# Kernel tuning notes

Measured on AMD Instinct MI355X. Metric: run time of the kernel, lower is better.

The kernel has to match this reference:

```python
import jax, jax.numpy as jnp
import numpy as np
from jax import lax

B, R, C, K = 4, 512, 80, 100          # images, rois/img, fg classes, post_nms_top_k
NMS_TH, SCORE_TH = 0.3, 0.1
MEAN = jnp.zeros(4, jnp.float32)       # delta_mean
STD = jnp.ones(4, jnp.float32)         # delta_std
NEG = jnp.float32(-1e9)
DWH_CLIP = jnp.float32(4.135166556742356)  # log(1000/16), standard bbox_xform clip


def setup_inputs() -> dict:
    key = jax.random.key(0)
    k1, k2, k3, k4 = jax.random.split(key, 4)
    x1y1 = jax.random.uniform(k1, (B, R, 2), minval=0.0, maxval=800.0)
    wh = jax.random.uniform(k2, (B, R, 2), minval=16.0, maxval=220.0)
    batch_rois = jnp.concatenate([x1y1, jnp.minimum(x1y1 + wh, 1023.0)], axis=-1)
    bbox_score = jax.random.uniform(k3, (B * R, C + 1, 1, 1), dtype=jnp.float32)
    bbox_deltas = jax.random.normal(k4, (B * R, (C + 1) * 4, 1, 1), dtype=jnp.float32) * 0.2
    im_hw = jnp.full((B, 1, 1, 2), 1024, dtype=jnp.int32)
    return {"batch_rois": batch_rois, "bbox_score": bbox_score,
            "bbox_deltas": bbox_deltas, "im_hw": im_hw}


def _pairwise_iou(b):
    # b: [R, 4] (x1,y1,x2,y2) -> [R, R]
    area = (b[:, 2] - b[:, 0]) * (b[:, 3] - b[:, 1])
    lt = jnp.maximum(b[:, None, :2], b[None, :, :2])
    rb = jnp.minimum(b[:, None, 2:], b[None, :, 2:])
    wh = jnp.maximum(rb - lt, 0.0)
    inter = wh[..., 0] * wh[..., 1]
    return inter / (area[:, None] + area[None, :] - inter + 1e-9)


def _nms_one_class(boxes, scores):
    # boxes: [R,4], scores: [R] -> keep mask + score-sorted boxes/scores
    order = jnp.argsort(-scores)
    b = boxes[order]
    s = scores[order]
    iou = _pairwise_iou(b)  # [R, R]

    def body(sup, i):
        keep_i = jnp.logical_and(jnp.logical_not(sup[i]), s[i] > SCORE_TH)
        new = jnp.where(keep_i, jnp.logical_or(sup, iou[i] > NMS_TH), sup)
        new = new.at[i].set(sup[i])  # never self-suppress
        return new, keep_i

    _, keep = lax.scan(body, jnp.zeros(b.shape[0], bool), jnp.arange(b.shape[0]))
    return keep, b, s


def _decode(rois, deltas, hw):
    # rois: [R,4], deltas: [R,C,4], hw: [2] (h, w) -> decoded boxes [R,C,4]
    d = deltas * STD + MEAN
    w = rois[:, 2] - rois[:, 0]
    h = rois[:, 3] - rois[:, 1]
    cx = rois[:, 0] + 0.5 * w
    cy = rois[:, 1] + 0.5 * h
    dx, dy = d[..., 0], d[..., 1]
    dw = jnp.minimum(d[..., 2], DWH_CLIP)
    dh = jnp.minimum(d[..., 3], DWH_CLIP)
    pcx = dx * w[:, None] + cx[:, None]
    pcy = dy * h[:, None] + cy[:, None]
    pw = w[:, None] * jnp.exp(dw)
    ph = h[:, None] * jnp.exp(dh)
    x1 = jnp.clip(pcx - 0.5 * pw, 0.0, hw[1] - 1.0)
    y1 = jnp.clip(pcy - 0.5 * ph, 0.0, hw[0] - 1.0)
    x2 = jnp.clip(pcx + 0.5 * pw, 0.0, hw[1] - 1.0)
    y2 = jnp.clip(pcy + 0.5 * ph, 0.0, hw[0] - 1.0)
    return jnp.stack([x1, y1, x2, y2], axis=-1)


def reference(batch_rois, bbox_score, bbox_deltas, im_hw):
    scores = bbox_score.reshape(B, R, C + 1)[..., 1:]               # [B,R,C] (skip bg)
    deltas = bbox_deltas.reshape(B, R, C + 1, 4)[:, :, 1:, :]       # [B,R,C,4]
    hw = im_hw.reshape(B, 2).astype(jnp.float32)

    def per_image(rois, sc, dl, hw_i):
        boxes = _decode(rois, dl, hw_i)                              # [R,C,4]
        keep, bs, ss = jax.vmap(_nms_one_class)(
            jnp.swapaxes(boxes, 0, 1), sc.T)                         # [C,R]...
        cls = jnp.broadcast_to(jnp.arange(C, dtype=jnp.float32)[:, None], (C, R))
        flat_s = jnp.where(keep, ss, NEG).reshape(-1)                # [C*R]
        top_s, idx = lax.top_k(flat_s, K)
        tb = bs.reshape(-1, 4)[idx]
        tc = cls.reshape(-1)[idx]
        valid = top_s > NEG * 0.5
        row = jnp.concatenate([tb, top_s[:, None], tc[:, None]], axis=-1)  # [K,6]
        pad = jnp.concatenate([jnp.zeros((K, 5), jnp.float32),
                               -jnp.ones((K, 1), jnp.float32)], axis=-1)
        return jnp.where(valid[:, None], row, pad)

    return jax.vmap(per_image)(batch_rois, scores, deltas, hw)      # [B,K,6]
```

## Files before the change

### kernel.cpp

```cpp
#include <hip/hip_runtime.h>
#include <cstdint>

#define BB 4
#define RR 512
#define CC 80
#define KK 100
#define NMS_TH 0.3f
#define SCORE_TH 0.1f
#define DWH_CLIP 4.135166556742356f

typedef unsigned short u16;
typedef unsigned int u32;
typedef unsigned long long u64;

__device__ __forceinline__ u32 f32_sortable(float f) {
  u32 u = __float_as_uint(f);
  u32 mask = (u32)((int)u >> 31) | 0x80000000u;
  return u ^ mask;
}
__device__ __forceinline__ float sortable_to_f32(u32 s) {
  u32 u = (s & 0x80000000u) ? (s ^ 0x80000000u) : ~s;
  return __uint_as_float(u);
}

__global__ __launch_bounds__(512) void nms_fused(
    const float* __restrict__ rois,
    const float* __restrict__ scores,
    const float* __restrict__ deltas,
    const int*   __restrict__ im_hw,
    u64*   __restrict__ cand_key,
    float4* __restrict__ cand_box)
{
#pragma clang fp contract(off)
  const int bc = blockIdx.x;
  const int b = bc / CC, c = bc % CC;
  const int tid = threadIdx.x;
  const int lane = tid & 63, wv = tid >> 6;

  __shared__ u64    keyarr[2 * RR];
  __shared__ float4 box_s[RR];
  __shared__ float  sco_s[RR];
  __shared__ u64    rmk_w[8 * 64];
  __shared__ u64    supacc_arr[8];
  __shared__ float4 kbox[KK];
  __shared__ float  ksc[KK];
  __shared__ float  karea[KK];
  __shared__ int    nkept_s;

  const float fh = (float)im_hw[b * 2 + 0] - 1.0f;
  const float fw = (float)im_hw[b * 2 + 1] - 1.0f;

  {
    const float sc = scores[(b * RR + tid) * (CC + 1) + (c + 1)];
    u64 v = ((u64)(~f32_sortable(sc)) << 32) | (u32)tid;
    const u32 t = (u32)tid;
    u32 pp = 0;
    for (u32 kk = 2; kk <= RR; kk <<= 1) {
      for (u32 j = kk >> 1; j > 0; j >>= 1) {
        u64 p;
        if (j >= 64) {
          u64* buf = keyarr + (pp & 1) * RR;
          buf[t] = v;
          __syncthreads();
          p = buf[t ^ j];
          ++pp;
        } else {
          p = __shfl_xor(v, (int)j);
        }
        bool up = ((t & kk) == 0);
        bool lower = ((t & j) == 0);
        bool takemin = (up == lower);
        bool pless = (p < v);
        v = (takemin == pless) ? p : v;
      }
    }
    keyarr[t] = v;
  }
  __syncthreads();

  {
    const u64 kv = keyarr[tid];
    const int r = (int)(kv & 0xFFFFFFFFull);
    const float sc = sortable_to_f32(~(u32)(kv >> 32));
    const float4 roi = *(const float4*)&rois[(b * RR + r) * 4];
    const int base = (b * RR + r) * (CC + 1) + (c + 1);
    const float4 d = *(const float4*)&deltas[base * 4];

    float w  = roi.z - roi.x;
    float h  = roi.w - roi.y;
    float cx = roi.x + 0.5f * w;
    float cy = roi.y + 0.5f * h;
    float dw = fminf(d.z, DWH_CLIP);
    float dh = fminf(d.w, DWH_CLIP);
    float pcx = d.x * w + cx;
    float pcy = d.y * h + cy;
    float pw = w * expf(dw);
    float ph = h * expf(dh);
    float hx = 0.5f * pw, hy = 0.5f * ph;
    float x1 = fminf(fmaxf(pcx - hx, 0.0f), fw);
    float y1 = fminf(fmaxf(pcy - hy, 0.0f), fh);
    float x2 = fminf(fmaxf(pcx + hx, 0.0f), fw);
    float y2 = fminf(fmaxf(pcy + hy, 0.0f), fh);

    box_s[tid] = make_float4(x1, y1, x2, y2);
    sco_s[tid] = sc;
    if (tid == 0) nkept_s = 0;
  }
  __syncthreads();

  int nk = 0;
  for (int w = 0; w < 8 && nk < KK; ++w) {
    const float4 bxc = box_s[w * 64 + lane];
    const float ar = (bxc.z - bxc.x) * (bxc.w - bxc.y);
    const float areps = ar + 1e-9f;

    {
      float4 cb[8]; float ca[8]; float inA[8];
      #pragma unroll
      for (int jj = 0; jj < 8; ++jj) {
        cb[jj] = box_s[w * 64 + wv * 8 + jj];
        ca[jj] = (cb[jj].z - cb[jj].x) * (cb[jj].w - cb[jj].y);
      }
      u64 myrow = 0;
      u32 unca = 0;
      #pragma unroll
      for (int jj = 0; jj < 8; ++jj) {
        float iw = fminf(bxc.z, cb[jj].z) - fmaxf(bxc.x, cb[jj].x);
        float ih = fminf(bxc.w, cb[jj].w) - fmaxf(bxc.y, cb[jj].y);
        iw = fmaxf(iw, 0.0f);
        ih = fmaxf(ih, 0.0f);
        const float inter = iw * ih;
        inA[jj] = inter;
        const float S = ca[jj] + areps;
        const bool yes = inter * 4.3333247f > S;
        const bool no  = inter * 4.3333420f < S;
        myrow |= yes ? (1ull << jj) : 0ull;
        unca  |= (!(yes || no)) ? (1u << jj) : 0u;
      }
      if (__any(unca != 0)) {
        #pragma unroll
        for (int jj = 0; jj < 8; ++jj) {
          const float denom = ((ca[jj] + ar) - inA[jj]) + 1e-9f;
          const bool pe = inA[jj] / denom > NMS_TH;
          const u64 bit = 1ull << jj;
          if (unca & (1u << jj)) myrow = pe ? (myrow | bit) : (myrow & ~bit);
        }
      }
      myrow <<= (wv * 8);
      myrow &= ~((2ull << lane) - 1ull);
      rmk_w[wv * 64 + lane] = myrow;
    }

    {
      bool sup = false, unca = false;
      for (int kx = wv; kx < nk; kx += 8) {
        const float4 kb = kbox[kx];
        const float ka = karea[kx];
        float iw = fminf(bxc.z, kb.z) - fmaxf(bxc.x, kb.x);
        float ih = fminf(bxc.w, kb.w) - fmaxf(bxc.y, kb.y);
        iw = fmaxf(iw, 0.0f);
        ih = fmaxf(ih, 0.0f);
        const float inter = iw * ih;
        const float S = ka + areps;
        const bool yes = inter * 4.3333247f > S;
        const bool no  = inter * 4.3333420f < S;
        sup  = sup  || yes;
        unca = unca || (!(yes || no));
      }
      if (__any(unca && !sup)) {
        sup = false;
        for (int kx = wv; kx < nk; kx += 8) {
          const float4 kb = kbox[kx];
          const float ka = karea[kx];
          float iw = fminf(bxc.z, kb.z) - fmaxf(bxc.x, kb.x);
          float ih = fminf(bxc.w, kb.w) - fmaxf(bxc.y, kb.y);
          iw = fmaxf(iw, 0.0f);
          ih = fmaxf(ih, 0.0f);
          const float inter = iw * ih;
          const float denom = ((ka + ar) - inter) + 1e-9f;
          sup = sup || (inter / denom > NMS_TH);
        }
      }
      const u64 bal = __ballot(sup);
      if (lane == 0) supacc_arr[wv] = bal;
    }
    __syncthreads();

    if (wv == 0) {
      u64 sup2 = supacc_arr[0];
      #pragma unroll
      for (int ww = 1; ww < 8; ++ww) sup2 |= supacc_arr[ww];
      u64 rm = rmk_w[lane];
      #pragma unroll
      for (int ww = 1; ww < 8; ++ww) rm |= rmk_w[ww * 64 + lane];
      const u32 rlo = (u32)rm, rhi = (u32)(rm >> 32);
      u64 todo = __ballot(sco_s[w * 64 + lane] > SCORE_TH) & ~sup2;
      int nkl = nk;
      while (todo) {
        const int i = __ffsll((long long)todo) - 1;
        if (lane == 0) {
          const float4 kb = box_s[w * 64 + i];
          kbox[nkl] = kb;
          ksc[nkl] = sco_s[w * 64 + i];
          karea[nkl] = (kb.z - kb.x) * (kb.w - kb.y);
        }
        ++nkl;
        if (nkl >= KK) break;
        const u32 rl = (u32)__builtin_amdgcn_readlane((int)rlo, i);
        const u32 rh = (u32)__builtin_amdgcn_readlane((int)rhi, i);
        todo &= ~((2ull << i) - 1ull);
        todo &= ~(((u64)rh << 32) | rl);
      }
      if (lane == 0) nkept_s = nkl;
    }
    __syncthreads();
    nk = nkept_s;
  }

  if (tid < KK) {
    const int kx = tid;
    u64 kv; float4 obx;
    if (kx < nk) {
      kv = ((u64)(~f32_sortable(ksc[kx])) << 32) | ((u64)(u32)c << 16) | (u32)kx;
      obx = kbox[kx];
    } else {
      kv = ((u64)(~f32_sortable(-1e9f)) << 32) | ((u64)(u32)c << 16) | (u32)kx;
      obx = make_float4(0.f, 0.f, 0.f, 0.f);
    }
    cand_key[bc * KK + kx] = kv;
    cand_box[bc * KK + kx] = obx;
  }
}

__device__ __forceinline__ void sort128(u64* smallkeys, int tid) {
  u64 v = (tid < 128) ? smallkeys[tid] : ~0ull;
  const u32 t = (u32)tid;
  for (u32 kk = 2; kk <= 128; kk <<= 1) {
    for (u32 j = kk >> 1; j > 0; j >>= 1) {
      if (j >= 64) {
        if (tid < 128) smallkeys[t] = v;
        __syncthreads();
        u64 p = (tid < 128) ? smallkeys[t ^ j] : ~0ull;
        __syncthreads();
        if (tid < 128) {
          bool up = ((t & kk) == 0);
          bool lower = ((t & j) == 0);
          bool takemin = (up == lower);
          bool pless = (p < v);
          v = (takemin == pless) ? p : v;
        }
      } else if (tid < 128) {
        u64 p = __shfl_xor(v, (int)j);
        bool up = ((t & kk) == 0);
        bool lower = ((t & j) == 0);
        bool takemin = (up == lower);
        bool pless = (p < v);
        v = (takemin == pless) ? p : v;
      }
    }
  }
  if (tid < 128) smallkeys[t] = v;
  __syncthreads();
}

__global__ __launch_bounds__(1024) void topk_select(
    const u64* __restrict__ cand_key,
    const float4* __restrict__ cand_box,
    float* __restrict__ out)
{
  const int b = blockIdx.x;
  const int tid = threadIdx.x;
  const int lane = tid & 63, wv = tid >> 6;
  const int N = CC * KK;
  const u64* __restrict__ keys_g = cand_key + (size_t)b * N;

  __shared__ u16 candA[CC * KK];
  __shared__ u16 candB[CC * KK];
  __shared__ u32 whist[16][256];
  __shared__ u32 bins[256];
  __shared__ u64 smallkeys[128];
  __shared__ int ncand_s, rank_s, q_s;
  __shared__ u32 cnt_s;

  if (tid == 0) { ncand_s = N; rank_s = KK - 1; }

  u16* cur = candA;
  u16* oth = candB;
  bool first = true;
  int d = 7;
  for (;;) {
    for (int t = tid; t < 16 * 256; t += 1024) ((u32*)whist)[t] = 0;
    __syncthreads();
    const int nc = first ? N : ncand_s;
    const int sh = d * 8;
    for (int t0 = 0; t0 < nc; t0 += 1024) {
      const int t = t0 + tid;
      if (t < nc) {
        const int idx = first ? t : (int)cur[t];
        u32 dig = (u32)((keys_g[idx] >> sh) & 0xFF);
        atomicAdd(&whist[wv][dig], 1u);
      }
    }
    __syncthreads();
    if (tid < 256) {
      u32 s = 0;
      #pragma unroll
      for (int w = 0; w < 16; ++w) s += whist[w][tid];
      bins[tid] = s;
    }
    __syncthreads();
    if (wv == 0) {
      u32 c0 = bins[lane * 4 + 0], c1 = bins[lane * 4 + 1];
      u32 c2 = bins[lane * 4 + 2], c3 = bins[lane * 4 + 3];
      u32 lsum = c0 + c1 + c2 + c3;
      u32 incl = lsum;
      #pragma unroll
      for (int off = 1; off < 64; off <<= 1) {
        u32 v = __shfl_up(incl, off);
        if (lane >= off) incl += v;
      }
      u32 excl = incl - lsum;
      int rk = rank_s;
      u32 s0 = excl, s1 = excl + c0, s2 = s1 + c1, s3 = s2 + c2;
      int q = -1; u32 nr = 0;
      if (rk >= (int)s0 && rk < (int)(s0 + c0)) { q = lane * 4 + 0; nr = rk - s0; }
      else if (rk >= (int)s1 && rk < (int)(s1 + c1)) { q = lane * 4 + 1; nr = rk - s1; }
      else if (rk >= (int)s2 && rk < (int)(s2 + c2)) { q = lane * 4 + 2; nr = rk - s2; }
      else if (rk >= (int)s3 && rk < (int)(s3 + c3)) { q = lane * 4 + 3; nr = rk - s3; }
      if (q >= 0) { q_s = q; rank_s = (int)nr; }
    }
    if (tid == 0) cnt_s = 0;
    __syncthreads();
    const int q = q_s;
    for (int t0 = 0; t0 < nc; t0 += 1024) {
      const int t = t0 + tid;
      int idx = 0; bool m = false;
      if (t < nc) {
        idx = first ? t : (int)cur[t];
        m = ((int)((keys_g[idx] >> sh) & 0xFF) == q);
      }
      u64 bal = __ballot(m);
      u32 base = 0;
      if (lane == 0 && bal) base = atomicAdd(&cnt_s, (u32)__popcll(bal));
      base = __shfl(base, 0);
      if (m) oth[base + (u32)__popcll(bal & ((1ull << lane) - 1ull))] = (u16)idx;
    }
    __syncthreads();
    if (tid == 0) ncand_s = (int)cnt_s;
    { u16* tmp = cur; cur = oth; oth = tmp; }
    first = false;
    __syncthreads();
    if (ncand_s <= 128 || d == 0) break;
    --d;
  }

  u64 T;
  const int nc2 = ncand_s;
  if (nc2 == 1) {
    T = keys_g[cur[0]];
  } else {
    if (tid < 128) smallkeys[tid] = (tid < nc2) ? keys_g[cur[tid]] : ~0ull;
    __syncthreads();
    sort128(smallkeys, tid);
    T = smallkeys[rank_s];
    __syncthreads();
  }

  if (tid == 0) cnt_s = 0;
  if (tid < 128) smallkeys[tid] = ~0ull;
  __syncthreads();
  for (int t0 = 0; t0 < N; t0 += 1024) {
    const int t = t0 + tid;
    u64 k = 0; bool m = false;
    if (t < N) { k = keys_g[t]; m = (k <= T); }
    u64 bal = __ballot(m);
    u32 base = 0;
    if (lane == 0 && bal) base = atomicAdd(&cnt_s, (u32)__popcll(bal));
    base = __shfl(base, 0);
    if (m) {
      u32 p = base + (u32)__popcll(bal & ((1ull << lane) - 1ull));
      if (p < 128) smallkeys[p] = k;
    }
  }
  __syncthreads();

  sort128(smallkeys, tid);

  if (tid < KK) {
    const u64 kv = smallkeys[tid];
    const float s = sortable_to_f32(~(u32)(kv >> 32));
    float x1 = 0.f, y1 = 0.f, x2 = 0.f, y2 = 0.f, so = 0.f, cf = -1.0f;
    if (s > -5.0e8f) {
      int c = (int)((kv >> 16) & 0xFFFFull);
      int k = (int)(kv & 0xFFFFull);
      float4 bx = cand_box[((size_t)b * CC + c) * KK + k];
      x1 = bx.x; y1 = bx.y; x2 = bx.z; y2 = bx.w;
      so = s; cf = (float)c;
    }
    float* o = out + ((size_t)b * KK + tid) * 6;
    o[0] = x1; o[1] = y1; o[2] = x2; o[3] = y2; o[4] = so; o[5] = cf;
  }
}

extern "C" void kernel_launch(void* const* d_in, const int* in_sizes, int n_in,
                              void* d_out, int out_size, void* d_ws, size_t ws_size,
                              hipStream_t stream) {
  (void)in_sizes; (void)n_in; (void)out_size; (void)ws_size;
  const float* rois   = (const float*)d_in[0];
  const float* scores = (const float*)d_in[1];
  const float* deltas = (const float*)d_in[2];
  const int*   im_hw  = (const int*)d_in[3];

  char* ws = (char*)d_ws;
  u64*    cand_key = (u64*)ws;
  float4* cand_box = (float4*)(ws + 256000);

  nms_fused<<<BB * CC, 512, 0, stream>>>(rois, scores, deltas, im_hw,
                                         cand_key, cand_box);
  topk_select<<<BB, 1024, 0, stream>>>(cand_key, cand_box, (float*)d_out);
}
```

Measured before the change: 62.15 us.

## Keep top-k radix-select keys in registers with per-thread candidate masks

The radix-select top-k kernel now loads each thread's eight candidate keys into registers once. Surviving candidates are tracked with a per-thread bitmask instead of compacting index lists into shared memory and re-reading keys from global memory on every digit pass. This removes the per-pass ballot compaction and the repeated global loads, and gets the candidate count straight from the histogram. In exchange it always does an extra sort128 pass to find the threshold and holds more registers per thread in a 1024-thread block.

```diff
diff --git a/kernel.cpp b/kernel.cpp
--- a/kernel.cpp
+++ b/kernel.cpp
@@ -274,30 +274,31 @@
   const int N = CC * KK;
   const u64* __restrict__ keys_g = cand_key + (size_t)b * N;
 
-  __shared__ u16 candA[CC * KK];
-  __shared__ u16 candB[CC * KK];
   __shared__ u32 whist[16][256];
   __shared__ u32 bins[256];
   __shared__ u64 smallkeys[128];
-  __shared__ int ncand_s, rank_s, q_s;
+  __shared__ int rank_s, q_s, ncand_s;
   __shared__ u32 cnt_s;
 
-  if (tid == 0) { ncand_s = N; rank_s = KK - 1; }
-
-  u16* cur = candA;
-  u16* oth = candB;
-  bool first = true;
+  u64 myk[8];
+  #pragma unroll
+  for (int i = 0; i < 8; ++i) {
+    const int t = i * 1024 + tid;
+    myk[i] = (t < N) ? keys_g[t] : ~0ull;
+  }
+  u32 mask8 = 0xFF;
+  if (tid == 0) rank_s = KK - 1;
+
   int d = 7;
+  int nc;
   for (;;) {
     for (int t = tid; t < 16 * 256; t += 1024) ((u32*)whist)[t] = 0;
     __syncthreads();
-    const int nc = first ? N : ncand_s;
-    const int sh = d * 8;
-    for (int t0 = 0; t0 < nc; t0 += 1024) {
-      const int t = t0 + tid;
-      if (t < nc) {
-        const int idx = first ? t : (int)cur[t];
-        u32 dig = (u32)((keys_g[idx] >> sh) & 0xFF);
+    const int sh = 8 * d;
+    #pragma unroll
+    for (int i = 0; i < 8; ++i) {
+      if (mask8 & (1u << i)) {
+        const u32 dig = (u32)((myk[i] >> sh) & 0xFF);
         atomicAdd(&whist[wv][dig], 1u);
       }
     }
@@ -310,80 +311,73 @@
     }
     __syncthreads();
     if (wv == 0) {
-      u32 c0 = bins[lane * 4 + 0], c1 = bins[lane * 4 + 1];
-      u32 c2 = bins[lane * 4 + 2], c3 = bins[lane * 4 + 3];
-      u32 lsum = c0 + c1 + c2 + c3;
+      const u32 c0 = bins[lane * 4 + 0], c1 = bins[lane * 4 + 1];
+      const u32 c2 = bins[lane * 4 + 2], c3 = bins[lane * 4 + 3];
+      const u32 lsum = c0 + c1 + c2 + c3;
       u32 incl = lsum;
       #pragma unroll
       for (int off = 1; off < 64; off <<= 1) {
-        u32 v = __shfl_up(incl, off);
+        const u32 v = __shfl_up(incl, off);
         if (lane >= off) incl += v;
       }
-      u32 excl = incl - lsum;
-      int rk = rank_s;
-      u32 s0 = excl, s1 = excl + c0, s2 = s1 + c1, s3 = s2 + c2;
-      int q = -1; u32 nr = 0;
-      if (rk >= (int)s0 && rk < (int)(s0 + c0)) { q = lane * 4 + 0; nr = rk - s0; }
-      else if (rk >= (int)s1 && rk < (int)(s1 + c1)) { q = lane * 4 + 1; nr = rk - s1; }
-      else if (rk >= (int)s2 && rk < (int)(s2 + c2)) { q = lane * 4 + 2; nr = rk - s2; }
-      else if (rk >= (int)s3 && rk < (int)(s3 + c3)) { q = lane * 4 + 3; nr = rk - s3; }
-      if (q >= 0) { q_s = q; rank_s = (int)nr; }
-    }
-    if (tid == 0) cnt_s = 0;
-    __syncthreads();
-    const int q = q_s;
-    for (int t0 = 0; t0 < nc; t0 += 1024) {
-      const int t = t0 + tid;
-      int idx = 0; bool m = false;
-      if (t < nc) {
-        idx = first ? t : (int)cur[t];
-        m = ((int)((keys_g[idx] >> sh) & 0xFF) == q);
-      }
-      u64 bal = __ballot(m);
-      u32 base = 0;
-      if (lane == 0 && bal) base = atomicAdd(&cnt_s, (u32)__popcll(bal));
-      base = __shfl(base, 0);
-      if (m) oth[base + (u32)__popcll(bal & ((1ull << lane) - 1ull))] = (u16)idx;
-    }
-    __syncthreads();
-    if (tid == 0) ncand_s = (int)cnt_s;
-    { u16* tmp = cur; cur = oth; oth = tmp; }
-    first = false;
-    __syncthreads();
-    if (ncand_s <= 128 || d == 0) break;
+      const u32 excl = incl - lsum;
+      const int rk = rank_s;
+      const u32 s0 = excl, s1 = excl + c0, s2 = s1 + c1, s3 = s2 + c2;
+      int q = -1; u32 nr = 0; u32 cnt = 0;
+      if (rk >= (int)s0 && rk < (int)(s0 + c0)) { q = lane * 4 + 0; nr = rk - s0; cnt = c0; }
+      else if (rk >= (int)s1 && rk < (int)(s1 + c1)) { q = lane * 4 + 1; nr = rk - s1; cnt = c1; }
+      else if (rk >= (int)s2 && rk < (int)(s2 + c2)) { q = lane * 4 + 2; nr = rk - s2; cnt = c2; }
+      else if (rk >= (int)s3 && rk < (int)(s3 + c3)) { q = lane * 4 + 3; nr = rk - s3; cnt = c3; }
+      if (q >= 0) { q_s = q; rank_s = (int)nr; ncand_s = (int)cnt; }
+    }
+    __syncthreads();
+    const u32 q = (u32)q_s;
+    nc = ncand_s;
+    #pragma unroll
+    for (int i = 0; i < 8; ++i) {
+      const u32 dig = (u32)((myk[i] >> sh) & 0xFF);
+      if (dig != q) mask8 &= ~(1u << i);
+    }
+    if (nc <= 128 || d == 0) break;
     --d;
-  }
-
-  u64 T;
-  const int nc2 = ncand_s;
-  if (nc2 == 1) {
-    T = keys_g[cur[0]];
-  } else {
-    if (tid < 128) smallkeys[tid] = (tid < nc2) ? keys_g[cur[tid]] : ~0ull;
-    __syncthreads();
-    sort128(smallkeys, tid);
-    T = smallkeys[rank_s];
-    __syncthreads();
   }
 
   if (tid == 0) cnt_s = 0;
   if (tid < 128) smallkeys[tid] = ~0ull;
   __syncthreads();
-  for (int t0 = 0; t0 < N; t0 += 1024) {
-    const int t = t0 + tid;
-    u64 k = 0; bool m = false;
-    if (t < N) { k = keys_g[t]; m = (k <= T); }
-    u64 bal = __ballot(m);
+  #pragma unroll
+  for (int i = 0; i < 8; ++i) {
+    const bool m = (mask8 & (1u << i)) != 0;
+    const u64 bal = __ballot(m);
     u32 base = 0;
     if (lane == 0 && bal) base = atomicAdd(&cnt_s, (u32)__popcll(bal));
     base = __shfl(base, 0);
     if (m) {
-      u32 p = base + (u32)__popcll(bal & ((1ull << lane) - 1ull));
-      if (p < 128) smallkeys[p] = k;
-    }
-  }
-  __syncthreads();
-
+      const u32 p = base + (u32)__popcll(bal & ((1ull << lane) - 1ull));
+      if (p < 128) smallkeys[p] = myk[i];
+    }
+  }
+  __syncthreads();
+  sort128(smallkeys, tid);
+  const u64 T = smallkeys[rank_s];
+  __syncthreads();
+
+  if (tid == 0) cnt_s = 0;
+  if (tid < 128) smallkeys[tid] = ~0ull;
+  __syncthreads();
+  #pragma unroll
+  for (int i = 0; i < 8; ++i) {
+    const bool m = (myk[i] <= T);
+    const u64 bal = __ballot(m);
+    u32 base = 0;
+    if (lane == 0 && bal) base = atomicAdd(&cnt_s, (u32)__popcll(bal));
+    base = __shfl(base, 0);
+    if (m) {
+      const u32 p = base + (u32)__popcll(bal & ((1ull << lane) - 1ull));
+      if (p < 128) smallkeys[p] = myk[i];
+    }
+  }
+  __syncthreads();
   sort128(smallkeys, tid);
 
   if (tid < KK) {
@@ -391,9 +385,9 @@
     const float s = sortable_to_f32(~(u32)(kv >> 32));
     float x1 = 0.f, y1 = 0.f, x2 = 0.f, y2 = 0.f, so = 0.f, cf = -1.0f;
     if (s > -5.0e8f) {
-      int c = (int)((kv >> 16) & 0xFFFFull);
-      int k = (int)(kv & 0xFFFFull);
-      float4 bx = cand_box[((size_t)b * CC + c) * KK + k];
+      const int c = (int)((kv >> 16) & 0xFFFFull);
+      const int k = (int)(kv & 0xFFFFull);
+      const float4 bx = cand_box[((size_t)b * CC + c) * KK + k];
       x1 = bx.x; y1 = bx.y; x2 = bx.z; y2 = bx.w;
       so = s; cf = (float)c;
     }
```

New measurement: 55.91 us. 1.11x faster.
